# Kernel tuning notes

Hardware: AMD Instinct MI355X
Metric: run time of the kernel (lower is better)

## Reference

```python
import jax, jax.numpy as jnp
import numpy as np
from jax.scipy.special import erf

B, S, D = 8, 512, 512
H = 8            # num_heads per half
DH = D // 2      # 256, per-branch model dim
DFF = 2048
HOUT = 2


def _layernorm(x, g, b, eps=1e-6):
    mu = jnp.mean(x, axis=-1, keepdims=True)
    var = jnp.mean(jnp.square(x - mu), axis=-1, keepdims=True)
    return (x - mu) / jnp.sqrt(var + eps) * g + b


def _rescale_dist(w):
    one = jnp.float32(1.0)
    return (one + jnp.exp(one)) / (one + jnp.exp(one - w))


def _mha(xin, wq, bq, wk, bk, wv, bv, wo, bo, maskf, adjoin, dist):
    b, s, dm = xin.shape
    dep = dm // H
    def heads(t):
        return t.reshape(b, s, H, dep).transpose(0, 2, 1, 3)  # (b,h,s,dep)
    q = heads(xin @ wq + bq)
    k = heads(xin @ wk + bk)
    v = heads(xin @ wv + bv)
    scores = jnp.einsum('bhqd,bhkd->bhqk', q, k)
    scale = jnp.sqrt(jnp.float32(dep))
    if dist is not None:
        scores = jax.nn.relu(scores) * _rescale_dist(dist) / scale
    else:
        scores = scores / scale
    scores = scores + maskf * jnp.float32(-1e9)
    if adjoin is not None:
        scores = scores + adjoin
    attn = jax.nn.softmax(scores, axis=-1)
    out = jnp.einsum('bhqk,bhkd->bhqd', attn, v).transpose(0, 2, 1, 3).reshape(b, s, dm)
    return out @ wo + bo, attn


def setup_inputs() -> dict:
    key = jax.random.key(0)
    ks = jax.random.split(key, 32)
    init = lambda k, shp: (jax.random.normal(k, shp, dtype=jnp.float32) * 0.02)
    inp = {
        'x': jax.random.normal(ks[0], (B, S, D), dtype=jnp.float32),
        'adjoin_matrix': jax.random.normal(ks[1], (B, 1, S, S), dtype=jnp.float32),
        'dist_matrix': jax.random.uniform(ks[2], (B, 1, S, S), dtype=jnp.float32),
        # mha1 (adjoin branch)
        'wq1': init(ks[3], (DH, DH)), 'bq1': jnp.zeros((DH,), jnp.float32),
        'wk1': init(ks[4], (DH, DH)), 'bk1': jnp.zeros((DH,), jnp.float32),
        'wv1': init(ks[5], (DH, DH)), 'bv1': jnp.zeros((DH,), jnp.float32),
        'wo1': init(ks[6], (DH, DH)), 'bo1': jnp.zeros((DH,), jnp.float32),
        # mha2 (distance branch)
        'wq2': init(ks[7], (DH, DH)), 'bq2': jnp.zeros((DH,), jnp.float32),
        'wk2': init(ks[8], (DH, DH)), 'bk2': jnp.zeros((DH,), jnp.float32),
        'wv2': init(ks[9], (DH, DH)), 'bv2': jnp.zeros((DH,), jnp.float32),
        'wo2': init(ks[10], (DH, DH)), 'bo2': jnp.zeros((DH,), jnp.float32),
        # BANLayer
        'vnet_w': init(ks[11], (DH, 2 * DH)), 'vnet_b': jnp.zeros((2 * DH,), jnp.float32),
        'qnet_w': init(ks[12], (DH, 2 * DH)), 'qnet_b': jnp.zeros((2 * DH,), jnp.float32),
        'h_mat': init(ks[13], (1, HOUT, 1, 2 * DH)),
        'h_bias': init(ks[14], (1, HOUT, 1, 1)),
        'bn_gamma': jnp.ones((D,), jnp.float32), 'bn_beta': jnp.zeros((D,), jnp.float32),
        'bn_mean': jnp.zeros((D,), jnp.float32), 'bn_var': jnp.ones((D,), jnp.float32),
        # LayerNorms
        'ln1_g': jnp.ones((D,), jnp.float32), 'ln1_b': jnp.zeros((D,), jnp.float32),
        'ln2_g': jnp.ones((D,), jnp.float32), 'ln2_b': jnp.zeros((D,), jnp.float32),
        # FFN
        'ffn_w1': init(ks[15], (D, DFF)), 'ffn_b1': jnp.zeros((DFF,), jnp.float32),
        'ffn_w2': init(ks[16], (DFF, D)), 'ffn_b2': jnp.zeros((D,), jnp.float32),
        # padding mask (int -> cast), 1 = masked
        'encoder_padding_mask': jax.random.randint(ks[17], (B, 1, 1, S), 0, 2, dtype=jnp.int32),
    }
    return inp


def reference(x, adjoin_matrix, dist_matrix,
              wq1, bq1, wk1, bk1, wv1, bv1, wo1, bo1,
              wq2, bq2, wk2, bk2, wv2, bv2, wo2, bo2,
              vnet_w, vnet_b, qnet_w, qnet_b, h_mat, h_bias,
              bn_gamma, bn_beta, bn_mean, bn_var,
              ln1_g, ln1_b, ln2_g, ln2_b,
              ffn_w1, ffn_b1, ffn_w2, ffn_b2,
              encoder_padding_mask):
    maskf = encoder_padding_mask.astype(jnp.float32)
    x1, x2 = jnp.split(x, 2, axis=-1)
    # local branch: adjoin bias, no distance
    x_l, aw_local = _mha(x1, wq1, bq1, wk1, bk1, wv1, bv1, wo1, bo1, maskf, adjoin_matrix, None)
    # global branch: relu + distance rescale, no adjoin
    x_g, aw_global = _mha(x2, wq2, bq2, wk2, bk2, wv2, bv2, wo2, bo2, maskf, None, dist_matrix)
    # BANLayer (h_out=2 <= c, eval mode; p_net is identity for rows=1)
    v_ = jax.nn.relu(x_l @ vnet_w + vnet_b)   # (B,S,2*DH)
    q_ = jax.nn.relu(x_g @ qnet_w + qnet_b)
    att_maps = jnp.einsum('xhyk,bvk,bqk->bhvq', h_mat, v_, q_) + h_bias  # (B,HOUT,S,S)
    logits = jnp.einsum('bvk,bhvq,bqk->bvk', v_, att_maps, q_)           # sum over h
    logits = (logits - bn_mean) / jnp.sqrt(bn_var + 1e-3) * bn_gamma + bn_beta
    attn_output = logits * jnp.concatenate([x_l, x_g], axis=-1)
    out1 = _layernorm(x + attn_output, ln1_g, ln1_b)
    h = out1 @ ffn_w1 + ffn_b1
    h = 0.5 * h * (1.0 + erf(h / jnp.sqrt(jnp.float32(2.0))))  # exact gelu
    ffn_out = h @ ffn_w2 + ffn_b2
    out2 = _layernorm(out1 + ffn_out, ln2_g, ln2_b)
    return (out2, aw_local, aw_global)
```

## Files before the change

### kernel.cpp

```cpp
#include <hip/hip_runtime.h>
#include <hip/hip_bf16.h>

typedef __hip_bfloat16 bf16;
typedef __attribute__((ext_vector_type(8))) short bf16x8;
typedef __attribute__((ext_vector_type(4))) float f32x4;
typedef __attribute__((ext_vector_type(4))) _Float16 f16x4;
typedef unsigned int u32;

#define BB 8
#define SS 512
#define DD 512
#define NH 8
#define DHm 256
#define DFF 2048

__device__ __forceinline__ void gl_lds16(const void* g, void* l) {
  __builtin_amdgcn_global_load_lds((const __attribute__((address_space(1))) void*)g,
                                   (__attribute__((address_space(3))) void*)l, 16, 0, 0);
}

__device__ __forceinline__ bf16x8 cvt8(const float* p) {
  union { bf16x8 v; bf16 h[8]; } u;
  float4 f0 = *(const float4*)p, f1 = *(const float4*)(p + 4);
  u.h[0]=__float2bfloat16(f0.x); u.h[1]=__float2bfloat16(f0.y);
  u.h[2]=__float2bfloat16(f0.z); u.h[3]=__float2bfloat16(f0.w);
  u.h[4]=__float2bfloat16(f1.x); u.h[5]=__float2bfloat16(f1.y);
  u.h[6]=__float2bfloat16(f1.z); u.h[7]=__float2bfloat16(f1.w);
  return u.v;
}

#define STAGE_G(buf, k0)                                                   \
  {                                                                        \
    _Pragma("unroll")                                                      \
    for (int j = 0; j < BM / 64; j++)                                      \
      gl_lds16(Ab + (long long)(srow + j * 64) * lda + (k0) + skc,         \
               (char*)As[buf] + wave * 1024 + j * 4096);                   \
    _Pragma("unroll")                                                      \
    for (int j = 0; j < BN / 64; j++)                                      \
      gl_lds16(Bb + (long long)(srow + j * 64) * ldb + (k0) + skc,         \
               (char*)Bs[buf] + wave * 1024 + j * 4096);                   \
  }

template<int BM, int BN, int SMODE, int BIASM, int ACT, int VTM>
__global__ __launch_bounds__(256)
void gemm2(const bf16* __restrict__ A, const bf16* __restrict__ B,
           const float* __restrict__ bias, float* __restrict__ Cf,
           bf16* __restrict__ Cb, int K, int lda, int ldb, int ldc,
           long long sA, long long sB, long long sC, int sBias,
           bf16* __restrict__ Cb2, const float* __restrict__ cscale)
{
  __shared__ bf16 As[2][BM * 32];
  __shared__ bf16 Bs[2][BN * 32];
  const int t = threadIdx.x, lane = t & 63, wave = t >> 6;
  const int l15 = lane & 15, quad = lane >> 4;
  constexpr int WMT = BM / 32, WNT = BN / 32;
  const int wm = (wave & 1) * (BM / 2), wn = (wave >> 1) * (BN / 2);
  const int row0 = blockIdx.y * BM, col0 = blockIdx.x * BN;
  const bf16* Ab = A + (long long)blockIdx.z * sA + (long long)row0 * lda;
  const bf16* Bb = B + (long long)blockIdx.z * sB + (long long)col0 * ldb;
  const int srow = wave * 16 + (lane >> 2), skc = (lane & 3) << 3;

  f32x4 acc[WMT][WNT] = {};

  STAGE_G(0, 0)
  asm volatile("s_waitcnt vmcnt(0)" ::: "memory");
  __builtin_amdgcn_s_barrier();

  int cur = 0;
  for (int k0 = 0; k0 < K; k0 += 32) {
    if (k0 + 32 < K) STAGE_G(cur ^ 1, k0 + 32)
    bf16x8 af[WMT], bfr[WNT];
#pragma unroll
    for (int i = 0; i < WMT; i++) af[i]  = *(const bf16x8*)&As[cur][(wm + i * 16 + l15) * 32 + quad * 8];
#pragma unroll
    for (int j = 0; j < WNT; j++) bfr[j] = *(const bf16x8*)&Bs[cur][(wn + j * 16 + l15) * 32 + quad * 8];
#pragma unroll
    for (int i = 0; i < WMT; i++)
#pragma unroll
      for (int j = 0; j < WNT; j++)
        acc[i][j] = __builtin_amdgcn_mfma_f32_16x16x32_bf16(af[i], bfr[j], acc[i][j], 0, 0, 0);
    asm volatile("s_waitcnt vmcnt(0)" ::: "memory");
    __builtin_amdgcn_s_barrier();
    cur ^= 1;
  }

  float sb = 0.f;
  if (BIASM == 2) sb = bias[0] + bias[1];
#pragma unroll
  for (int i = 0; i < WMT; i++)
#pragma unroll
    for (int j = 0; j < WNT; j++) {
      int col = col0 + wn + j * 16 + l15;
      float bv = (BIASM == 1) ? bias[(long long)blockIdx.z * sBias + col] : sb;
      float vv[4];
#pragma unroll
      for (int r = 0; r < 4; r++) {
        float v = acc[i][j][r] + bv;
        if (ACT == 1) v = fmaxf(v, 0.f);
        if (ACT == 2) v = 0.5f * v * (1.f + erff(v * 0.70710678118654752f));
        vv[r] = v;
      }
      const int rowb = row0 + wm + i * 16 + (quad << 2);
      if (VTM == 1) {
        const int bidx = rowb >> 9, kpos = rowb & 511;
        const long long zz8 = (long long)blockIdx.z * 8 + bidx;
        if (col < 512) {
          const int part = col >> 8, hh = (col >> 5) & 7, dep = col & 31;
          bf16* dst = Cb2 + (((zz8 * 8 + hh) * 2 + part) * 512 + (long long)kpos) * 32 + dep;
#pragma unroll
          for (int r = 0; r < 4; r++) dst[r * 32] = __float2bfloat16(vv[r]);
        } else {
          const int hh = (col - 512) >> 5, dep = (col - 512) & 31;
          long long vo = ((zz8 * 8 + hh) * 64 + (kpos >> 3)) * 32 + dep;
          bf16 h0 = __float2bfloat16(vv[0]), h1 = __float2bfloat16(vv[1]);
          bf16 h2 = __float2bfloat16(vv[2]), h3 = __float2bfloat16(vv[3]);
          short4 pk;
          pk.x = *(short*)&h0; pk.y = *(short*)&h1; pk.z = *(short*)&h2; pk.w = *(short*)&h3;
          *(short4*)(Cb + vo * 8 + (kpos & 7)) = pk;
        }
      } else {
#pragma unroll
        for (int r = 0; r < 4; r++) {
          long long ci = (long long)blockIdx.z * sC + (long long)(rowb + r) * ldc + col;
          if (SMODE & 1) Cf[ci] = vv[r];
          if (SMODE & 2) Cb[ci] = __float2bfloat16(vv[r]);
          if (VTM == 2) Cb2[ci] = __float2bfloat16(vv[r] * cscale[col]);
        }
      }
    }
}

__global__ __launch_bounds__(256, 2)
void attn_fused(const bf16* __restrict__ QKF, const bf16* __restrict__ VT,
                const int* __restrict__ mask, const _Float16* __restrict__ EP,
                float* __restrict__ awl, float* __restrict__ awg,
                bf16* __restrict__ ctx1, bf16* __restrict__ ctx2)
{
  const int qt = blockIdx.x, h = blockIdx.y, zz = blockIdx.z;
  const int b = zz & 7, branch = zz >> 3;
  float* __restrict__ aw = branch ? awg : awl;
  bf16* __restrict__ ctx = branch ? ctx2 : ctx1;

  const int t = threadIdx.x, lane = t & 63, wave = t >> 6;
  const int l15 = lane & 15, quad = lane >> 4;
  __shared__ bf16x8 Vt[64][32];
  alignas(16) __shared__ bf16 Pl[4][2048];
  __shared__ float mvalf[512];

  const bf16* VTs = VT + ((long long)zz * 8 + h) * 16384;
#pragma unroll
  for (int j = 0; j < 8; j++)
    gl_lds16(VTs + (long long)t * 8 + j * 2048, (char*)Vt + wave * 1024 + j * 4096);

  { int2 m2 = *(const int2*)(mask + b * SS + t * 2);
    mvalf[t * 2]     = (float)m2.x * -1e9f;
    mvalf[t * 2 + 1] = (float)m2.y * -1e9f; }

  const int q0 = qt * 64 + wave * 16;
  const bf16* Qbase = QKF + ((long long)zz * 8 + h) * 2 * 16384;
  const bf16* Kbase = Qbase + 16384;
  bf16x8 qfrag = *(const bf16x8*)(Qbase + (long long)(q0 + l15) * 32 + quad * 8);
  __syncthreads();

  const float scale_inv = 0.17677669529663688f;
  const f16x4* Ep = (const f16x4*)EP + (((long long)zz * 8 + qt) * 4 + wave) * 2048;

  u32 eh[64];
  float rsum[4] = {0.f, 0.f, 0.f, 0.f};
  f32x4 oacc[2] = {};
  short* Pw = (short*)Pl[wave];
  const int rkey = ((l15 >> 2) ^ l15) & 3;

#pragma unroll
  for (int c = 0; c < 4; c++) {
#pragma unroll
    for (int kcl = 0; kcl < 8; kcl++) {
      const int kc = c * 8 + kcl;
      const int kpos = kc * 16 + l15;
      bf16x8 kfrag = *(const bf16x8*)(Kbase + (long long)kpos * 32 + quad * 8);
      f16x4 e4 = Ep[kc * 64 + lane];
      f32x4 a = __builtin_amdgcn_mfma_f32_16x16x32_bf16(qfrag, kfrag, f32x4{0.f,0.f,0.f,0.f}, 0, 0, 0);
      float mv = (branch == 0) ? 0.f : mvalf[kpos];
      u32 p01 = 0, p23 = 0;
#pragma unroll
      for (int r = 0; r < 4; r++) {
        float s = (branch == 0) ? fmaf(a[r], scale_inv, (float)e4[r])
                                : fmaf(fmaxf(a[r], 0.f), (float)e4[r], mv);
        float e = __expf(s);
        rsum[r] += e;
        u32 xb = __float_as_uint(e);
        u32 b16 = (xb + 0x7FFFu + ((xb >> 16) & 1u)) >> 16;
        if (r == 0)      p01 = b16;
        else if (r == 1) p01 |= b16 << 16;
        else if (r == 2) p23 = b16;
        else             p23 |= b16 << 16;
        const int key = (quad ^ r) & 3;
        const int off = (quad * 4 + r) * 256 + (((kcl * 16 + l15) * 2) ^ (key << 5));
        *(short*)((char*)Pw + off) = (short)b16;
      }
      eh[kc * 2]     = p01;
      eh[kc * 2 + 1] = p23;
    }
    __builtin_amdgcn_s_setprio(1);
#pragma unroll
    for (int k2 = 0; k2 < 4; k2++) {
      const int off = l15 * 256 + ((k2 * 64 + quad * 16) ^ (rkey << 5));
      bf16x8 afr = *(const bf16x8*)((const char*)Pw + off);
      const int blk = (c * 4 + k2) * 4 + quad;
      oacc[0] = __builtin_amdgcn_mfma_f32_16x16x32_bf16(afr, Vt[blk][l15],      oacc[0], 0, 0, 0);
      oacc[1] = __builtin_amdgcn_mfma_f32_16x16x32_bf16(afr, Vt[blk][16 + l15], oacc[1], 0, 0, 0);
    }
    __builtin_amdgcn_s_setprio(0);
  }

  float rsi[4];
#pragma unroll
  for (int r = 0; r < 4; r++) {
    float v = rsum[r];
    v += __shfl_xor(v, 1, 16);
    v += __shfl_xor(v, 2, 16);
    v += __shfl_xor(v, 4, 16);
    v += __shfl_xor(v, 8, 16);
    rsi[r] = 1.f / v;
  }

#pragma unroll
  for (int n = 0; n < 2; n++)
#pragma unroll
    for (int r = 0; r < 4; r++) {
      int q = q0 + quad * 4 + r;
      ctx[(long long)(b * SS + q) * DHm + h * 32 + n * 16 + l15] =
          __float2bfloat16(oacc[n][r] * rsi[r]);
    }

  float* awp = aw + (((long long)(b * NH + h) * SS + q0)) * SS;
#pragma unroll
  for (int kc = 0; kc < 32; kc++) {
    u32 p01 = eh[kc * 2], p23 = eh[kc * 2 + 1];
#pragma unroll
    for (int r = 0; r < 4; r++) {
      u32 bits = (r == 0) ? (p01 & 0xFFFFu) : (r == 1) ? (p01 >> 16)
               : (r == 2) ? (p23 & 0xFFFFu) : (p23 >> 16);
      float e = __uint_as_float(bits << 16);
      awp[(long long)(quad * 4 + r) * SS + kc * 16 + l15] = e * rsi[r];
    }
  }
}

__device__ __forceinline__ void tr_tile(const float* __restrict__ src, bf16* __restrict__ dst,
                                        int K, int N, int tile) {
  __shared__ float tl[32][33];
  int tilesN = N >> 5;
  int tk = tile / tilesN, tn = tile % tilesN;
  int c = threadIdx.x & 31, r0 = threadIdx.x >> 5;
#pragma unroll
  for (int i = 0; i < 4; i++) {
    int r = r0 + i * 8;
    tl[r][c] = src[(long long)(tk * 32 + r) * N + tn * 32 + c];
  }
  __syncthreads();
#pragma unroll
  for (int i = 0; i < 4; i++) {
    int r = r0 + i * 8;
    dst[(long long)(tn * 32 + r) * K + tk * 32 + c] = __float2bfloat16(tl[c][r]);
  }
}

__global__ __launch_bounds__(256)
void pack_all(const float* wq1, const float* wk1, const float* wv1,
              const float* wq2, const float* wk2, const float* wv2,
              const float* wo1, const float* wo2,
              const float* vnet_w, const float* qnet_w,
              const float* ffn_w1, const float* ffn_w2,
              const float* bq1, const float* bk1, const float* bv1,
              const float* bq2, const float* bk2, const float* bv2,
              const float* bo1, const float* bo2,
              const float* vnet_b, const float* qnet_b,
              const float* h_mat,
              const float* x,
              const float* adjoin, const float* dist, const int* mask,
              bf16* WB1, bf16* WB2, bf16* woT1, bf16* woT2,
              bf16* vnetT, bf16* qnetT, bf16* f1T, bf16* f2T,
              float* BB1v, float* BB2v, float* BOv, float* VQb, float* HSv,
              bf16* xb, _Float16* EP)
{
  int blk = blockIdx.x;
  if (blk < 64)        { tr_tile(wq1, WB1,            256, 256, blk); return; }
  if (blk < 128)       { tr_tile(wk1, WB1 + 256*256,  256, 256, blk-64); return; }
  if (blk < 192)       { tr_tile(wv1, WB1 + 512*256,  256, 256, blk-128); return; }
  if (blk < 256)       { tr_tile(wq2, WB2,            256, 256, blk-192); return; }
  if (blk < 320)       { tr_tile(wk2, WB2 + 256*256,  256, 256, blk-256); return; }
  if (blk < 384)       { tr_tile(wv2, WB2 + 512*256,  256, 256, blk-320); return; }
  if (blk < 448)       { tr_tile(wo1, woT1,           256, 256, blk-384); return; }
  if (blk < 512)       { tr_tile(wo2, woT2,           256, 256, blk-448); return; }
  if (blk < 640)       { tr_tile(vnet_w, vnetT,       256, 512, blk-512); return; }
  if (blk < 768)       { tr_tile(qnet_w, qnetT,       256, 512, blk-640); return; }
  if (blk < 1792)      { tr_tile(ffn_w1, f1T,         512, 2048, blk-768); return; }
  if (blk < 2816)      { tr_tile(ffn_w2, f2T,         2048, 512, blk-1792); return; }
  if (blk < 3840) {
    long long i0 = (long long)(blk - 2816) * 2048 + threadIdx.x * 8;
    *(bf16x8*)(xb + i0) = cvt8(x + i0);
    return;
  }
  if (blk < 3846) {
    int b = blk - 3840;
    const float* src = b==0?bq1 : b==1?bk1 : b==2?bv1 : b==3?bq2 : b==4?bk2 : bv2;
    float* dst = (b < 3 ? BB1v : BB2v) + (b % 3) * 256;
    dst[threadIdx.x] = src[threadIdx.x];
    return;
  }
  if (blk < 3848) {
    int b = blk - 3846;
    BOv[b * 256 + threadIdx.x] = (b ? bo2 : bo1)[threadIdx.x];
    return;
  }
  if (blk < 3852) {
    int b = blk - 3848;
    const float* src = (b < 2) ? vnet_b : qnet_b;
    VQb[b * 256 + threadIdx.x] = src[(b & 1) * 256 + threadIdx.x];
    return;
  }
  if (blk < 3853) {
    int t = threadIdx.x;
    HSv[t]       = h_mat[t]       + h_mat[512 + t];
    HSv[t + 256] = h_mat[256 + t] + h_mat[768 + t];
    return;
  }
  {
    const int e = blk - 3853;
    const int qt = e & 7, kt = (e >> 3) & 3, zz = e >> 5;
    const int b = zz & 7, branch = zz >> 3;
    const float* E = (branch ? dist : adjoin) + ((long long)b * SS + qt * 64) * SS + kt * 128;
    __shared__ float tile[64][129];
    const int t = threadIdx.x;
    const int r0 = t >> 5, c4 = (t & 31) * 4;
#pragma unroll
    for (int jj = 0; jj < 8; jj++) {
      int row = r0 + jj * 8;
      float4 f = *(const float4*)(E + (long long)row * SS + c4);
      tile[row][c4 + 0] = f.x; tile[row][c4 + 1] = f.y;
      tile[row][c4 + 2] = f.z; tile[row][c4 + 3] = f.w;
    }
    __syncthreads();
    const int lane = t & 63, wq = t >> 6, l15 = lane & 15, quad = lane >> 4;
    const float scale_inv = 0.17677669529663688f;
    f16x4* out = (f16x4*)EP;
#pragma unroll
    for (int kcl = 0; kcl < 8; kcl++) {
      int kk = kcl * 16 + l15;
      f16x4 o;
      if (branch == 0) {
        float mv = (float)mask[b * SS + kt * 128 + kk] * -1e9f;
#pragma unroll
        for (int r = 0; r < 4; r++)
          o[r] = (_Float16)(tile[wq * 16 + quad * 4 + r][kk] + mv);
      } else {
#pragma unroll
        for (int r = 0; r < 4; r++) {
          float ev = tile[wq * 16 + quad * 4 + r][kk];
          o[r] = (_Float16)(3.7182818284590452f / (1.f + __expf(1.f - ev)) * scale_inv);
        }
      }
      out[((((long long)zz * 8 + qt) * 4 + wq) * 32 + (kt * 8 + kcl)) * 64 + lane] = o;
    }
  }
}

__global__ __launch_bounds__(256)
void tr_qn(const bf16* __restrict__ Qn, bf16* __restrict__ QnT)
{
  int b = blockIdx.z, tk = blockIdx.y, tn = blockIdx.x;
  __shared__ bf16 tl[32][33];
  int c = threadIdx.x & 31, r0 = threadIdx.x >> 5;
  const bf16* src = Qn + (long long)b * 512 * 512;
  bf16* dst = QnT + (long long)b * 512 * 512;
#pragma unroll
  for (int i = 0; i < 4; i++) { int r = r0 + i * 8; tl[r][c] = src[(tk * 32 + r) * 512 + tn * 32 + c]; }
  __syncthreads();
#pragma unroll
  for (int i = 0; i < 4; i++) { int r = r0 + i * 8; dst[(tn * 32 + r) * 512 + tk * 32 + c] = tl[c][r]; }
}

__global__ __launch_bounds__(256)
void bn_gate_ln1_kernel(const float* __restrict__ x, const bf16* __restrict__ vbuf,
                        const float* __restrict__ T, const float* __restrict__ xl,
                        const float* __restrict__ xg,
                        const float* __restrict__ bng, const float* __restrict__ bnb,
                        const float* __restrict__ bnm, const float* __restrict__ bnv,
                        const float* __restrict__ lng, const float* __restrict__ lnb,
                        float* __restrict__ out1, bf16* __restrict__ out1b)
{
  const int row = blockIdx.x;
  const int t = threadIdx.x;
  const int lane = t & 63, wave = t >> 6;
  __shared__ float red[8];
  float val[2];
#pragma unroll
  for (int i = 0; i < 2; i++) {
    int c = t + i * 256;
    long long idx = (long long)row * DD + c;
    float lg = __bfloat162float(vbuf[idx]) * T[idx];
    float bn = (lg - bnm[c]) / sqrtf(bnv[c] + 1e-3f) * bng[c] + bnb[c];
    float gate = (c < DHm) ? xl[(long long)row * DHm + c] : xg[(long long)row * DHm + (c - DHm)];
    val[i] = x[idx] + bn * gate;
  }
  float s = val[0] + val[1];
#pragma unroll
  for (int o = 32; o > 0; o >>= 1) s += __shfl_xor(s, o);
  if (lane == 0) red[wave] = s;
  __syncthreads();
  float mu = (red[0] + red[1] + red[2] + red[3]) * (1.f / 512.f);
  float d0 = val[0] - mu, d1 = val[1] - mu;
  float vs = d0 * d0 + d1 * d1;
#pragma unroll
  for (int o = 32; o > 0; o >>= 1) vs += __shfl_xor(vs, o);
  if (lane == 0) red[4 + wave] = vs;
  __syncthreads();
  float inv = 1.f / sqrtf((red[4] + red[5] + red[6] + red[7]) * (1.f / 512.f) + 1e-6f);
  float o0 = d0 * inv * lng[t] + lnb[t];
  float o1 = d1 * inv * lng[t + 256] + lnb[t + 256];
  out1[(long long)row * DD + t] = o0;
  out1[(long long)row * DD + t + 256] = o1;
  out1b[(long long)row * DD + t] = __float2bfloat16(o0);
  out1b[(long long)row * DD + t + 256] = __float2bfloat16(o1);
}

__global__ __launch_bounds__(256)
void ln2_kernel(const float* __restrict__ a, const float* __restrict__ b2,
                const float* __restrict__ g, const float* __restrict__ bta,
                float* __restrict__ out)
{
  const int row = blockIdx.x;
  const int t = threadIdx.x;
  const int lane = t & 63, wave = t >> 6;
  __shared__ float red[8];
  float v0 = a[(long long)row * DD + t]       + b2[(long long)row * DD + t];
  float v1 = a[(long long)row * DD + t + 256] + b2[(long long)row * DD + t + 256];
  float s = v0 + v1;
#pragma unroll
  for (int o = 32; o > 0; o >>= 1) s += __shfl_xor(s, o);
  if (lane == 0) red[wave] = s;
  __syncthreads();
  float mu = (red[0] + red[1] + red[2] + red[3]) * (1.f / 512.f);
  float d0 = v0 - mu, d1 = v1 - mu;
  float vs = d0 * d0 + d1 * d1;
#pragma unroll
  for (int o = 32; o > 0; o >>= 1) vs += __shfl_xor(vs, o);
  if (lane == 0) red[4 + wave] = vs;
  __syncthreads();
  float inv = 1.f / sqrtf((red[4] + red[5] + red[6] + red[7]) * (1.f / 512.f) + 1e-6f);
  out[(long long)row * DD + t]       = d0 * inv * g[t]       + bta[t];
  out[(long long)row * DD + t + 256] = d1 * inv * g[t + 256] + bta[t + 256];
}

extern "C" void kernel_launch(void* const* d_in, const int* in_sizes, int n_in,
                              void* d_out, int out_size, void* d_ws, size_t ws_size,
                              hipStream_t stream) {
  const float* x      = (const float*)d_in[0];
  const float* adjoin = (const float*)d_in[1];
  const float* dist   = (const float*)d_in[2];
  const float* wq1=(const float*)d_in[3],  *bq1=(const float*)d_in[4];
  const float* wk1=(const float*)d_in[5],  *bk1=(const float*)d_in[6];
  const float* wv1=(const float*)d_in[7],  *bv1=(const float*)d_in[8];
  const float* wo1=(const float*)d_in[9],  *bo1=(const float*)d_in[10];
  const float* wq2=(const float*)d_in[11], *bq2=(const float*)d_in[12];
  const float* wk2=(const float*)d_in[13], *bk2=(const float*)d_in[14];
  const float* wv2=(const float*)d_in[15], *bv2=(const float*)d_in[16];
  const float* wo2=(const float*)d_in[17], *bo2=(const float*)d_in[18];
  const float* vnet_w=(const float*)d_in[19], *vnet_b=(const float*)d_in[20];
  const float* qnet_w=(const float*)d_in[21], *qnet_b=(const float*)d_in[22];
  const float* h_mat=(const float*)d_in[23], *h_bias=(const float*)d_in[24];
  const float* bn_g=(const float*)d_in[25], *bn_b=(const float*)d_in[26];
  const float* bn_m=(const float*)d_in[27], *bn_v=(const float*)d_in[28];
  const float* ln1_g=(const float*)d_in[29], *ln1_b=(const float*)d_in[30];
  const float* ln2_g=(const float*)d_in[31], *ln2_b=(const float*)d_in[32];
  const float* ffn_w1=(const float*)d_in[33], *ffn_b1=(const float*)d_in[34];
  const float* ffn_w2=(const float*)d_in[35], *ffn_b2=(const float*)d_in[36];
  const int* mask = (const int*)d_in[37];

  char* base = (char*)d_ws;
  size_t off = 0;
  auto alloc = [&](size_t bytes) { char* p = base + off; off += (bytes + 255) & ~(size_t)255; return p; };
  bf16*  xb    = (bf16*) alloc(4096LL*512*2);
  bf16*  WB1   = (bf16*) alloc(768*256*2);
  bf16*  WB2   = (bf16*) alloc(768*256*2);
  float* BB1v  = (float*)alloc(768*4);
  float* BB2v  = (float*)alloc(768*4);
  float* BOv   = (float*)alloc(512*4);
  float* VQb   = (float*)alloc(1024*4);
  float* HSv   = (float*)alloc(512*4);
  bf16*  woT1  = (bf16*) alloc(256*256*2);
  bf16*  woT2  = (bf16*) alloc(256*256*2);
  bf16*  vnetT = (bf16*) alloc(512*256*2);
  bf16*  qnetT = (bf16*) alloc(512*256*2);
  bf16*  f1T   = (bf16*) alloc(2048*512*2);
  bf16*  f2T   = (bf16*) alloc(512*2048*2);
  bf16*  QKF   = (bf16*) alloc(16LL*8*2*512*32*2);
  bf16*  VTb   = (bf16*) alloc(2LL*8*8*512*32*2);
  _Float16* EP = (_Float16*)alloc(8388608);
  bf16*  CTX   = (bf16*) alloc(4096LL*256*2);
  bf16*  CTX2  = (bf16*) alloc(4096LL*256*2);
  float* XL    = (float*)alloc(4096LL*256*4);
  float* XG    = (float*)alloc(4096LL*256*4);
  bf16*  XLb   = (bf16*) alloc(4096LL*256*2);
  bf16*  XGb   = (bf16*) alloc(4096LL*256*2);
  bf16*  Vn    = (bf16*) alloc(4096LL*512*2);
  bf16*  Qn    = (bf16*) alloc(4096LL*512*2);
  bf16*  QnT   = (bf16*) alloc(4096LL*512*2);
  bf16*  VH    = (bf16*) alloc(4096LL*512*2);
  bf16*  G     = (bf16*) alloc(8LL*512*512*2);
  float* T     = (float*)alloc(4096LL*512*4);
  float* OUT1  = (float*)alloc(4096LL*512*4);
  bf16*  OUT1b = (bf16*) alloc(4096LL*512*2);
  bf16*  H     = (bf16*) alloc(4096LL*2048*2);
  float* FFNO  = (float*)alloc(4096LL*512*4);

  float* out2 = (float*)d_out;
  float* awl  = out2 + 2097152LL;
  float* awg  = awl + 16777216LL;

  const int MR = BB * SS;
  const long long GST = (long long)SS * SS;

  pack_all<<<dim3(4365), 256, 0, stream>>>(
      wq1, wk1, wv1, wq2, wk2, wv2, wo1, wo2, vnet_w, qnet_w, ffn_w1, ffn_w2,
      bq1, bk1, bv1, bq2, bk2, bv2, bo1, bo2, vnet_b, qnet_b, h_mat, x,
      adjoin, dist, mask,
      WB1, WB2, woT1, woT2, vnetT, qnetT, f1T, f2T, BB1v, BB2v, BOv, VQb, HSv,
      xb, EP);

  gemm2<128,128,0,1,0,1><<<dim3(6, 32, 2), 256, 0, stream>>>(
      xb, WB1, BB1v, nullptr, VTb, 256, 512, 256, 768,
      256LL, 768LL*256, 0LL, 768, QKF, nullptr);

  attn_fused<<<dim3(8, NH, 16), 256, 0, stream>>>(
      QKF, VTb, mask, EP, awl, awg, CTX, CTX2);

  gemm2<64,64,3,1,0,0><<<dim3(4, 64, 2), 256, 0, stream>>>(
      CTX, woT1, BOv, XL, XLb, 256, 256, 256, 256,
      4096LL*256, 256LL*256, 4096LL*256, 256, nullptr, nullptr);

  gemm2<64,64,2,1,1,2><<<dim3(8, 64, 2), 256, 0, stream>>>(
      XLb, vnetT, VQb, nullptr, Vn, 256, 256, 256, 512,
      4096LL*256, 512LL*256, 4096LL*512, 512, VH, HSv);

  tr_qn<<<dim3(16, 16, BB), 256, 0, stream>>>(Qn, QnT);
  gemm2<64,64,2,2,0,0><<<dim3(8, 8, BB), 256, 0, stream>>>(
      VH, Qn, h_bias, nullptr, G, 512, 512, 512, 512, GST, GST, GST, 0, nullptr, nullptr);
  gemm2<64,64,1,0,0,0><<<dim3(8, 8, BB), 256, 0, stream>>>(
      G, QnT, nullptr, T, nullptr, 512, 512, 512, 512, GST, GST, GST, 0, nullptr, nullptr);

  bn_gate_ln1_kernel<<<dim3(MR), 256, 0, stream>>>(
      x, Vn, T, XL, XG, bn_g, bn_b, bn_m, bn_v, ln1_g, ln1_b, OUT1, OUT1b);

  gemm2<128,128,2,1,2,0><<<dim3(16, 32, 1), 256, 0, stream>>>(
      OUT1b, f1T, ffn_b1, nullptr, H, 512, 512, 512, 2048, 0, 0, 0, 0, nullptr, nullptr);
  gemm2<64,64,1,1,0,0><<<dim3(8, 64, 1), 256, 0, stream>>>(
      H, f2T, ffn_b2, FFNO, nullptr, 2048, 2048, 2048, 512, 0, 0, 0, 0, nullptr, nullptr);

  ln2_kernel<<<dim3(MR), 256, 0, stream>>>(OUT1, FFNO, ln2_g, ln2_b, out2);
}
```

Before: 444.4 us.

## Double K-step per GEMM iteration and fuse Qn transpose into vnet/qnet epilogue

The GEMM main loop now stages 64 K elements per barrier, as two 32-wide LDS sub-tiles, which halves the number of waitcnt/barrier synchronisations per tile at the cost of doubled LDS usage. The separate tr_qn transpose kernel is removed. The qnet branch of the vnet/qnet GEMM now writes its bf16 output tile into reused LDS and stores it transposed as QnT with vectorised writes. This drops one kernel launch and one read and write pass over Qn. The larger LDS footprint may reduce occupancy for the 128x128 GEMMs.

```diff
diff --git a/kernel.cpp b/kernel.cpp
--- a/kernel.cpp
+++ b/kernel.cpp
@@ -29,16 +29,22 @@
   return u.v;
 }
 
-#define STAGE_G(buf, k0)                                                   \
+#define STAGE2(buf, k0)                                                    \
   {                                                                        \
     _Pragma("unroll")                                                      \
-    for (int j = 0; j < BM / 64; j++)                                      \
+    for (int j = 0; j < BM / 64; j++) {                                    \
       gl_lds16(Ab + (long long)(srow + j * 64) * lda + (k0) + skc,         \
-               (char*)As[buf] + wave * 1024 + j * 4096);                   \
+               (char*)As[buf][0] + wave * 1024 + j * 4096);                \
+      gl_lds16(Ab + (long long)(srow + j * 64) * lda + (k0) + 32 + skc,    \
+               (char*)As[buf][1] + wave * 1024 + j * 4096);                \
+    }                                                                      \
     _Pragma("unroll")                                                      \
-    for (int j = 0; j < BN / 64; j++)                                      \
+    for (int j = 0; j < BN / 64; j++) {                                    \
       gl_lds16(Bb + (long long)(srow + j * 64) * ldb + (k0) + skc,         \
-               (char*)Bs[buf] + wave * 1024 + j * 4096);                   \
+               (char*)Bs[buf][0] + wave * 1024 + j * 4096);                \
+      gl_lds16(Bb + (long long)(srow + j * 64) * ldb + (k0) + 32 + skc,    \
+               (char*)Bs[buf][1] + wave * 1024 + j * 4096);                \
+    }                                                                      \
   }
 
 template<int BM, int BN, int SMODE, int BIASM, int ACT, int VTM>
@@ -47,10 +53,11 @@
            const float* __restrict__ bias, float* __restrict__ Cf,
            bf16* __restrict__ Cb, int K, int lda, int ldb, int ldc,
            long long sA, long long sB, long long sC, int sBias,
-           bf16* __restrict__ Cb2, const float* __restrict__ cscale)
+           bf16* __restrict__ Cb2, const float* __restrict__ cscale,
+           bf16* __restrict__ Cb3)
 {
-  __shared__ bf16 As[2][BM * 32];
-  __shared__ bf16 Bs[2][BN * 32];
+  __shared__ bf16 As[2][2][BM * 32];
+  __shared__ bf16 Bs[2][2][BN * 32];
   const int t = threadIdx.x, lane = t & 63, wave = t >> 6;
   const int l15 = lane & 15, quad = lane >> 4;
   constexpr int WMT = BM / 32, WNT = BN / 32;
@@ -62,23 +69,26 @@
 
   f32x4 acc[WMT][WNT] = {};
 
-  STAGE_G(0, 0)
+  STAGE2(0, 0)
   asm volatile("s_waitcnt vmcnt(0)" ::: "memory");
   __builtin_amdgcn_s_barrier();
 
   int cur = 0;
-  for (int k0 = 0; k0 < K; k0 += 32) {
-    if (k0 + 32 < K) STAGE_G(cur ^ 1, k0 + 32)
-    bf16x8 af[WMT], bfr[WNT];
-#pragma unroll
-    for (int i = 0; i < WMT; i++) af[i]  = *(const bf16x8*)&As[cur][(wm + i * 16 + l15) * 32 + quad * 8];
-#pragma unroll
-    for (int j = 0; j < WNT; j++) bfr[j] = *(const bf16x8*)&Bs[cur][(wn + j * 16 + l15) * 32 + quad * 8];
-#pragma unroll
-    for (int i = 0; i < WMT; i++)
-#pragma unroll
-      for (int j = 0; j < WNT; j++)
-        acc[i][j] = __builtin_amdgcn_mfma_f32_16x16x32_bf16(af[i], bfr[j], acc[i][j], 0, 0, 0);
+  for (int k0 = 0; k0 < K; k0 += 64) {
+    if (k0 + 64 < K) STAGE2(cur ^ 1, k0 + 64)
+#pragma unroll
+    for (int p = 0; p < 2; p++) {
+      bf16x8 af[WMT], bfr[WNT];
+#pragma unroll
+      for (int i = 0; i < WMT; i++) af[i]  = *(const bf16x8*)&As[cur][p][(wm + i * 16 + l15) * 32 + quad * 8];
+#pragma unroll
+      for (int j = 0; j < WNT; j++) bfr[j] = *(const bf16x8*)&Bs[cur][p][(wn + j * 16 + l15) * 32 + quad * 8];
+#pragma unroll
+      for (int i = 0; i < WMT; i++)
+#pragma unroll
+        for (int j = 0; j < WNT; j++)
+          acc[i][j] = __builtin_amdgcn_mfma_f32_16x16x32_bf16(af[i], bfr[j], acc[i][j], 0, 0, 0);
+    }
     asm volatile("s_waitcnt vmcnt(0)" ::: "memory");
     __builtin_amdgcn_s_barrier();
     cur ^= 1;
@@ -86,6 +96,7 @@
 
   float sb = 0.f;
   if (BIASM == 2) sb = bias[0] + bias[1];
+  bf16 (*tl)[65] = (bf16(*)[65])As;
 #pragma unroll
   for (int i = 0; i < WMT; i++)
 #pragma unroll
@@ -122,12 +133,29 @@
 #pragma unroll
         for (int r = 0; r < 4; r++) {
           long long ci = (long long)blockIdx.z * sC + (long long)(rowb + r) * ldc + col;
+          bf16 hb = __float2bfloat16(vv[r]);
           if (SMODE & 1) Cf[ci] = vv[r];
-          if (SMODE & 2) Cb[ci] = __float2bfloat16(vv[r]);
-          if (VTM == 2) Cb2[ci] = __float2bfloat16(vv[r] * cscale[col]);
+          if (SMODE & 2) Cb[ci] = hb;
+          if (VTM == 2) {
+            if (blockIdx.z == 0) Cb2[ci] = __float2bfloat16(vv[r] * cscale[col]);
+            else tl[wm + i * 16 + (quad << 2) + r][wn + j * 16 + l15] = hb;
+          }
         }
       }
     }
+
+  if (VTM == 2 && blockIdx.z == 1) {
+    __syncthreads();
+    const int o_r = t >> 2;
+    const int jb = (t & 3) * 16;
+    const int bidx = row0 >> 9;
+    bf16* dst = Cb3 + (long long)bidx * 262144 + (long long)(col0 + o_r) * 512 + (row0 & 511) + jb;
+    union { bf16x8 v; bf16 h[8]; } u0, u1;
+#pragma unroll
+    for (int j = 0; j < 8; j++) { u0.h[j] = tl[jb + j][o_r]; u1.h[j] = tl[jb + 8 + j][o_r]; }
+    *(bf16x8*)dst = u0.v;
+    *(bf16x8*)(dst + 8) = u1.v;
+  }
 }
 
 __global__ __launch_bounds__(256, 2)
@@ -364,21 +392,6 @@
       out[((((long long)zz * 8 + qt) * 4 + wq) * 32 + (kt * 8 + kcl)) * 64 + lane] = o;
     }
   }
-}
-
-__global__ __launch_bounds__(256)
-void tr_qn(const bf16* __restrict__ Qn, bf16* __restrict__ QnT)
-{
-  int b = blockIdx.z, tk = blockIdx.y, tn = blockIdx.x;
-  __shared__ bf16 tl[32][33];
-  int c = threadIdx.x & 31, r0 = threadIdx.x >> 5;
-  const bf16* src = Qn + (long long)b * 512 * 512;
-  bf16* dst = QnT + (long long)b * 512 * 512;
-#pragma unroll
-  for (int i = 0; i < 4; i++) { int r = r0 + i * 8; tl[r][c] = src[(tk * 32 + r) * 512 + tn * 32 + c]; }
-  __syncthreads();
-#pragma unroll
-  for (int i = 0; i < 4; i++) { int r = r0 + i * 8; dst[(tn * 32 + r) * 512 + tk * 32 + c] = tl[c][r]; }
 }
 
 __global__ __launch_bounds__(256)
@@ -531,32 +544,31 @@
 
   gemm2<128,128,0,1,0,1><<<dim3(6, 32, 2), 256, 0, stream>>>(
       xb, WB1, BB1v, nullptr, VTb, 256, 512, 256, 768,
-      256LL, 768LL*256, 0LL, 768, QKF, nullptr);
+      256LL, 768LL*256, 0LL, 768, QKF, nullptr, nullptr);
 
   attn_fused<<<dim3(8, NH, 16), 256, 0, stream>>>(
       QKF, VTb, mask, EP, awl, awg, CTX, CTX2);
 
   gemm2<64,64,3,1,0,0><<<dim3(4, 64, 2), 256, 0, stream>>>(
       CTX, woT1, BOv, XL, XLb, 256, 256, 256, 256,
-      4096LL*256, 256LL*256, 4096LL*256, 256, nullptr, nullptr);
+      4096LL*256, 256LL*256, 4096LL*256, 256, nullptr, nullptr, nullptr);
 
   gemm2<64,64,2,1,1,2><<<dim3(8, 64, 2), 256, 0, stream>>>(
       XLb, vnetT, VQb, nullptr, Vn, 256, 256, 256, 512,
-      4096LL*256, 512LL*256, 4096LL*512, 512, VH, HSv);
-
-  tr_qn<<<dim3(16, 16, BB), 256, 0, stream>>>(Qn, QnT);
+      4096LL*256, 512LL*256, 4096LL*512, 512, VH, HSv, QnT);
+
   gemm2<64,64,2,2,0,0><<<dim3(8, 8, BB), 256, 0, stream>>>(
-      VH, Qn, h_bias, nullptr, G, 512, 512, 512, 512, GST, GST, GST, 0, nullptr, nullptr);
+      VH, Qn, h_bias, nullptr, G, 512, 512, 512, 512, GST, GST, GST, 0, nullptr, nullptr, nullptr);
   gemm2<64,64,1,0,0,0><<<dim3(8, 8, BB), 256, 0, stream>>>(
-      G, QnT, nullptr, T, nullptr, 512, 512, 512, 512, GST, GST, GST, 0, nullptr, nullptr);
+      G, QnT, nullptr, T, nullptr, 512, 512, 512, 512, GST, GST, GST, 0, nullptr, nullptr, nullptr);
 
   bn_gate_ln1_kernel<<<dim3(MR), 256, 0, stream>>>(
       x, Vn, T, XL, XG, bn_g, bn_b, bn_m, bn_v, ln1_g, ln1_b, OUT1, OUT1b);
 
   gemm2<128,128,2,1,2,0><<<dim3(16, 32, 1), 256, 0, stream>>>(
-      OUT1b, f1T, ffn_b1, nullptr, H, 512, 512, 512, 2048, 0, 0, 0, 0, nullptr, nullptr);
+      OUT1b, f1T, ffn_b1, nullptr, H, 512, 512, 512, 2048, 0, 0, 0, 0, nullptr, nullptr, nullptr);
   gemm2<64,64,1,1,0,0><<<dim3(8, 64, 1), 256, 0, stream>>>(
-      H, f2T, ffn_b2, FFNO, nullptr, 2048, 2048, 2048, 512, 0, 0, 0, 0, nullptr, nullptr);
+      H, f2T, ffn_b2, FFNO, nullptr, 2048, 2048, 2048, 512, 0, 0, 0, 0, nullptr, nullptr, nullptr);
 
   ln2_kernel<<<dim3(MR), 256, 0, stream>>>(OUT1, FFNO, ln2_g, ln2_b, out2);
 }
```

Measured after the change: 491.1 us. 1.11x slower.
